# Kernel optimization log

Hardware: AMD Instinct MI355X
Metric: run time of the kernel (lower is better)

Reference implementation:

```python
import jax, jax.numpy as jnp
import numpy as np

B = 256        # graphs
NODES = 116    # nodes per view per graph
FEAT = 115     # node feature dim
LENN = 6670    # edges per view per graph (116*115/2)
SEG2 = 13456   # raw edges per graph in input (2*LENN + 116 discarded)
HID = 128      # hidden_channels
HC = 512       # hc


def setup_inputs() -> dict:
    key = jax.random.key(0)
    ks = jax.random.split(key, 12)
    x = jax.random.normal(ks[0], (B * 2 * NODES, FEAT), jnp.float32)
    # per-graph edge layout: [6670 FC edges | 6670 SC edges | 116 dummy]
    off = (2 * NODES) * jnp.arange(B, dtype=jnp.int32)  # [B]
    fc = jax.random.randint(ks[1], (2, B, LENN), 0, NODES, dtype=jnp.int32) + off[None, :, None]
    sc = jax.random.randint(ks[2], (2, B, LENN), 0, NODES, dtype=jnp.int32) + off[None, :, None] + NODES
    dummy = jnp.zeros((2, B, SEG2 - 2 * LENN), jnp.int32) + off[None, :, None]
    edge_index = jnp.concatenate([fc, sc, dummy], axis=2).reshape(2, B * SEG2)
    edge_weight = jax.random.uniform(ks[3], (B * SEG2,), jnp.float32)
    batch = jnp.repeat(jnp.arange(B, dtype=jnp.int32), 2 * NODES)
    s = 1.0 / np.sqrt(FEAT)
    W1 = jax.random.uniform(ks[4], (FEAT, HID), jnp.float32, -s, s)
    b1 = jnp.zeros((HID,), jnp.float32)
    W2 = jax.random.uniform(ks[5], (FEAT, HID), jnp.float32, -s, s)
    b2 = jnp.zeros((HID,), jnp.float32)
    s6 = 1.0 / np.sqrt(2 * NODES)
    W6 = jax.random.uniform(ks[6], (2 * NODES, HC), jnp.float32, -s6, s6)
    b6 = jax.random.uniform(ks[7], (HC,), jnp.float32, -s6, s6)
    s7 = 1.0 / np.sqrt(HC)
    W7 = jax.random.uniform(ks[8], (HC, 1), jnp.float32, -s7, s7)
    b7 = jax.random.uniform(ks[9], (1,), jnp.float32, -s7, s7)
    return dict(x=x, edge_index=edge_index, edge_weight=edge_weight, batch=batch,
                W1=W1, b1=b1, W2=W2, b2=b2, W6=W6, b6=b6, W7=W7, b7=b7)


def _gcn_conv(x, ei, ew, W, b, num_nodes):
    """PyG GCNConv: D^-1/2 (A+I) D^-1/2 X W + b (self-loop weight 1)."""
    h = x @ W                                   # [N, HID]
    src, dst = ei[0], ei[1]
    deg = jax.ops.segment_sum(ew, dst, num_segments=num_nodes) + 1.0  # +1 self-loop
    dinv = jax.lax.rsqrt(deg)                   # [N]
    norm = dinv[src] * ew * dinv[dst]           # [E]
    out = jax.ops.segment_sum(h[src] * norm[:, None], dst, num_segments=num_nodes)
    out = out + (dinv * dinv)[:, None] * h      # self-loop message
    return out + b


def reference(x, edge_index, edge_weight, batch, W1, b1, W2, b2, W6, b6, W7, b7):
    gidx = jnp.arange(B, dtype=edge_index.dtype)
    ei = edge_index.reshape(2, B, SEG2)
    ew = edge_weight.reshape(B, SEG2)
    # de-offset per-graph edges into per-view node index spaces (116 nodes/graph)
    ei_fc = (ei[:, :, :LENN] - NODES * gidx[None, :, None]).reshape(2, B * LENN)
    ei_sc = (ei[:, :, LENN:2 * LENN] - NODES * (gidx + 1)[None, :, None]).reshape(2, B * LENN)
    ew_fc = ew[:, :LENN].reshape(-1)
    ew_sc = ew[:, LENN:2 * LENN].reshape(-1)
    xr = x.reshape(B, 2 * NODES, FEAT)
    node_fc = xr[:, :NODES].reshape(B * NODES, FEAT)
    node_sc = xr[:, NODES:].reshape(B * NODES, FEAT)
    N = B * NODES
    x1 = _gcn_conv(node_fc, ei_fc, ew_fc, W1, b1, N).max(axis=1)  # [B*116]
    x2 = _gcn_conv(node_sc, ei_sc, ew_sc, W2, b2, N).max(axis=1)  # [B*116]
    feat = jnp.stack([x1, x2], axis=1).reshape(B, 2 * NODES)      # flatten()
    # dropout p=0.5 is identity in eval mode
    h = jax.nn.relu(feat @ W6 + b6)
    return h @ W7 + b7  # [B, 1]
```

## Files before the change

kernel.cpp:

```cpp
#include <hip/hip_runtime.h>


#define NB 256
#define NODES 116
#define FEAT 115
#define LENN 6670
#define SEG2 13456
#define HID 128
#define HC 512
#define AF_STR 117

typedef float f32x4 __attribute__((ext_vector_type(4)));
typedef short short8 __attribute__((ext_vector_type(8)));
typedef __bf16 bf16x8 __attribute__((ext_vector_type(8)));

#define MFMA16(a, b, c) __builtin_amdgcn_mfma_f32_16x16x32_bf16( \
    __builtin_bit_cast(bf16x8, (a)), __builtin_bit_cast(bf16x8, (b)), (c), 0, 0, 0)

#define OFF_ALO 32768
#define OFF_BHI 65536
#define OFF_BLO 98304
#define OFF_PMAX 131072
#define OFF_DINV 133120
#define LDS_BYTES 133632

__device__ __forceinline__ unsigned short f2bf_s(float f) {
  return __builtin_bit_cast(unsigned short, (__bf16)f);
}
__device__ __forceinline__ float bf2f_s(unsigned short h) {
  return __builtin_bit_cast(float, (unsigned)h << 16);
}
__device__ __forceinline__ void cvt4(const float* v, uint2& hi, uint2& lo) {
  unsigned short h[4], l[4];
#pragma unroll
  for (int j = 0; j < 4; ++j) {
    h[j] = f2bf_s(v[j]);
    l[j] = f2bf_s(v[j] - bf2f_s(h[j]));
  }
  hi.x = (unsigned)h[0] | ((unsigned)h[1] << 16);
  hi.y = (unsigned)h[2] | ((unsigned)h[3] << 16);
  lo.x = (unsigned)l[0] | ((unsigned)l[1] << 16);
  lo.y = (unsigned)l[2] | ((unsigned)l[3] << 16);
}
__device__ __forceinline__ int kperm(int k) {
  return (k & ~31) | (k & 3) | (((k >> 2) & 3) << 3) | (((k >> 4) & 1) << 2);
}
__device__ __forceinline__ int kb64(int t) {
  return ((t & 3) << 4) | (((t >> 2) & 1) << 3) | ((t >> 3) << 6);
}
__device__ __forceinline__ int swzb(int row, int kbyte) {
  return row * 256 + (kbyte ^ ((row & 7) << 4));
}
__device__ __forceinline__ f32x4 splat4(float f) {
  f32x4 r = {f, f, f, f};
  return r;
}

__global__ __launch_bounds__(1024, 1) void k_fused(
    const float* __restrict__ x, const int* __restrict__ ei,
    const float* __restrict__ ew,
    const float* __restrict__ W1, const float* __restrict__ b1,
    const float* __restrict__ W2, const float* __restrict__ b2,
    float* __restrict__ featws)
{
  __shared__ __align__(16) char sm[LDS_BYTES];
  float* Afp   = (float*)(sm + OFF_BHI);
  float* dinv  = (float*)(sm + OFF_DINV);
  float* pmaxp = (float*)(sm + OFF_PMAX);
  const int bid = blockIdx.x;
  const int g = bid >> 1, v = bid & 1;
  const int tid = threadIdx.x;

  {
    f32x4 z = splat4(0.f);
    f32x4* p = (f32x4*)(sm + OFF_BHI);
    for (int i = tid; i < 3393; i += 1024) p[i] = z;
  }
  __syncthreads();

  const int eoff = g * SEG2 + v * LENN;
  const int nbase = g * 232 + v * 116;

  {
    const int* __restrict__ srcp = ei + eoff;
    const int* __restrict__ dstp = ei + (size_t)NB * SEG2 + eoff;
    const float* __restrict__ wp = ew + eoff;
    for (int q = tid; q < (LENN / 2); q += 1024) {
      int2 s2 = ((const int2*)srcp)[q];
      int2 d2 = ((const int2*)dstp)[q];
      float2 w2 = ((const float2*)wp)[q];
      atomicAdd(&Afp[(d2.x - nbase) * AF_STR + (s2.x - nbase)], w2.x);
      atomicAdd(&Afp[(d2.y - nbase) * AF_STR + (s2.y - nbase)], w2.y);
    }
  }
  __syncthreads();

  if (tid < 4 * NODES) {
    const int r = tid >> 2, q = tid & 3;
    const float* row = Afp + r * AF_STR + q * 29;
    float s = 0.f;
#pragma unroll
    for (int j = 0; j < 29; ++j) s += row[j];
    s += __shfl_xor(s, 1, 64);
    s += __shfl_xor(s, 2, 64);
    if (q == 0) dinv[r] = rsqrtf(s + 1.0f);
  }
  __syncthreads();

  float xr[4][4];
  {
    const float* __restrict__ xg = x + (size_t)nbase * FEAT;
#pragma unroll
    for (int i = 0; i < 4; ++i) {
      int u = tid + (i << 10);
      int t = u >> 7, c = u & 127;
#pragma unroll
      for (int j = 0; j < 4; ++j) {
        int s = 4 * t + j;
        xr[i][j] = (c < FEAT && s < NODES) ? xg[s * FEAT + c] : 0.f;
      }
    }
  }

  for (int p = tid; p < NODES * 32; p += 1024) {
    const int row = p >> 5;
    const int t = p & 31;
    const int c = t << 2;
    float tv[4] = {0.f, 0.f, 0.f, 0.f};
    if (t < 29) {
      const float dr = dinv[row];
#pragma unroll
      for (int j = 0; j < 4; ++j) {
        const int cc = c + j;
        float q = Afp[row * AF_STR + cc] * (dr * dinv[cc]);
        if (cc == row) q += dr * dr;
        tv[j] = q;
      }
    }
    uint2 hi, lo;
    cvt4(tv, hi, lo);
    const int byte = swzb(row, kb64(t));
    *(uint2*)(sm + byte) = hi;
    *(uint2*)(sm + OFF_ALO + byte) = lo;
  }
  __syncthreads();

#pragma unroll
  for (int i = 0; i < 4; ++i) {
    int u = tid + (i << 10);
    int t = u >> 7, c = u & 127;
    uint2 hi, lo;
    cvt4(xr[i], hi, lo);
    int byte = swzb(c, kb64(t));
    *(uint2*)(sm + OFF_BHI + byte) = hi;
    *(uint2*)(sm + OFF_BLO + byte) = lo;
  }
  __syncthreads();

  const int lane = tid & 63, w = tid >> 6;
  const int mg = w >> 2, ng = w & 3;
  const int rA0 = (mg << 5) + (lane & 15), rA1 = rA0 + 16;
  const int rB0 = (ng << 5) + (lane & 15), rB1 = rB0 + 16;
  const int kb = (lane >> 4) << 4;

  float wr[4][4];
  {
    const float* __restrict__ Wv = v ? W2 : W1;
#pragma unroll
    for (int i = 0; i < 4; ++i) {
      int u = tid + (i << 10);
      int t = u >> 7, c = u & 127;
#pragma unroll
      for (int j = 0; j < 4; ++j) {
        int k = 4 * t + j;
        wr[i][j] = (k < FEAT) ? Wv[(size_t)k * HID + c] : 0.f;
      }
    }
  }

  f32x4 acc00 = splat4(0.f), acc01 = splat4(0.f);
  f32x4 acc10 = splat4(0.f), acc11 = splat4(0.f);

#pragma unroll
  for (int kc = 0; kc < 4; ++kc) {
    const int ko = (kc << 6) + kb;
    short8 a0h = *(const short8*)(sm + swzb(rA0, ko));
    short8 a0l = *(const short8*)(sm + OFF_ALO + swzb(rA0, ko));
    short8 a1h = *(const short8*)(sm + swzb(rA1, ko));
    short8 a1l = *(const short8*)(sm + OFF_ALO + swzb(rA1, ko));
    short8 b0h = *(const short8*)(sm + OFF_BHI + swzb(rB0, ko));
    short8 b0l = *(const short8*)(sm + OFF_BLO + swzb(rB0, ko));
    short8 b1h = *(const short8*)(sm + OFF_BHI + swzb(rB1, ko));
    short8 b1l = *(const short8*)(sm + OFF_BLO + swzb(rB1, ko));
    acc00 = MFMA16(a0h, b0h, acc00); acc00 = MFMA16(a0l, b0h, acc00); acc00 = MFMA16(a0h, b0l, acc00);
    acc01 = MFMA16(a0h, b1h, acc01); acc01 = MFMA16(a0l, b1h, acc01); acc01 = MFMA16(a0h, b1l, acc01);
    acc10 = MFMA16(a1h, b0h, acc10); acc10 = MFMA16(a1l, b0h, acc10); acc10 = MFMA16(a1h, b0l, acc10);
    acc11 = MFMA16(a1h, b1h, acc11); acc11 = MFMA16(a1l, b1h, acc11); acc11 = MFMA16(a1h, b1l, acc11);
  }
  __syncthreads();

  {
#pragma unroll
    for (int mt = 0; mt < 2; ++mt)
#pragma unroll
      for (int nt = 0; nt < 2; ++nt)
#pragma unroll
        for (int r2 = 0; r2 < 4; ++r2) {
          f32x4 a = (mt == 0) ? (nt == 0 ? acc00 : acc01)
                              : (nt == 0 ? acc10 : acc11);
          float f = a[r2];
          int row = (mg << 5) + (mt << 4) + ((lane >> 4) << 2) + r2;
          int col = (ng << 5) + (nt << 4) + (lane & 15);
          unsigned short hi = f2bf_s(f);
          unsigned short lo = f2bf_s(f - bf2f_s(hi));
          int byte = swzb(row, kperm(col) << 1);
          *(unsigned short*)(sm + byte) = hi;
          *(unsigned short*)(sm + OFF_ALO + byte) = lo;
        }
#pragma unroll
    for (int i = 0; i < 4; ++i) {
      int u = tid + (i << 10);
      int t = u >> 7, c = u & 127;
      uint2 hi, lo;
      cvt4(wr[i], hi, lo);
      int byte = swzb(c, kb64(t));
      *(uint2*)(sm + OFF_BHI + byte) = hi;
      *(uint2*)(sm + OFF_BLO + byte) = lo;
    }
  }
  __syncthreads();

  {
    const float* __restrict__ bv = v ? b2 : b1;
    float bb0 = bv[(ng << 5) + (lane & 15)];
    float bb1 = bv[(ng << 5) + 16 + (lane & 15)];
    acc00 = splat4(bb0); acc01 = splat4(bb1);
    acc10 = splat4(bb0); acc11 = splat4(bb1);
  }
#pragma unroll
  for (int kc = 0; kc < 4; ++kc) {
    const int ko = (kc << 6) + kb;
    short8 a0h = *(const short8*)(sm + swzb(rA0, ko));
    short8 a0l = *(const short8*)(sm + OFF_ALO + swzb(rA0, ko));
    short8 a1h = *(const short8*)(sm + swzb(rA1, ko));
    short8 a1l = *(const short8*)(sm + OFF_ALO + swzb(rA1, ko));
    short8 b0h = *(const short8*)(sm + OFF_BHI + swzb(rB0, ko));
    short8 b0l = *(const short8*)(sm + OFF_BLO + swzb(rB0, ko));
    short8 b1h = *(const short8*)(sm + OFF_BHI + swzb(rB1, ko));
    short8 b1l = *(const short8*)(sm + OFF_BLO + swzb(rB1, ko));
    acc00 = MFMA16(a0h, b0h, acc00); acc00 = MFMA16(a0l, b0h, acc00); acc00 = MFMA16(a0h, b0l, acc00);
    acc01 = MFMA16(a0h, b1h, acc01); acc01 = MFMA16(a0l, b1h, acc01); acc01 = MFMA16(a0h, b1l, acc01);
    acc10 = MFMA16(a1h, b0h, acc10); acc10 = MFMA16(a1l, b0h, acc10); acc10 = MFMA16(a1h, b0l, acc10);
    acc11 = MFMA16(a1h, b1h, acc11); acc11 = MFMA16(a1l, b1h, acc11); acc11 = MFMA16(a1h, b1l, acc11);
  }

#pragma unroll
  for (int mt = 0; mt < 2; ++mt)
#pragma unroll
    for (int r2 = 0; r2 < 4; ++r2) {
      f32x4 aN0 = (mt == 0) ? acc00 : acc10;
      f32x4 aN1 = (mt == 0) ? acc01 : acc11;
      float m = fmaxf(aN0[r2], aN1[r2]);
      m = fmaxf(m, __shfl_xor(m, 1, 64));
      m = fmaxf(m, __shfl_xor(m, 2, 64));
      m = fmaxf(m, __shfl_xor(m, 4, 64));
      m = fmaxf(m, __shfl_xor(m, 8, 64));
      if ((lane & 15) == 0) {
        int row = (mg << 5) + (mt << 4) + ((lane >> 4) << 2) + r2;
        pmaxp[(ng << 7) + row] = m;
      }
    }
  __syncthreads();
  if (tid < NODES) {
    float m = fmaxf(fmaxf(pmaxp[tid], pmaxp[128 + tid]),
                    fmaxf(pmaxp[256 + tid], pmaxp[384 + tid]));
    featws[g * 232 + 2 * tid + v] = m;
  }
}

__global__ __launch_bounds__(1024) void k_mlp(
    const float* __restrict__ featws, const float* __restrict__ W6,
    const float* __restrict__ b6, const float* __restrict__ W7,
    const float* __restrict__ b7, float* __restrict__ out)
{
  __shared__ float sf[232];
  __shared__ float ph[512];
  __shared__ float red[8];
  const int g = blockIdx.x, tid = threadIdx.x;
  if (tid < 232) sf[tid] = featws[g * 232 + tid];
  __syncthreads();

  const int col = tid & 511, half = tid >> 9;
  const float* __restrict__ w6p = W6 + (size_t)(half * 116) * HC + col;
  const float* __restrict__ sfh = sf + half * 116;
  float p = 0.f;
#pragma unroll 4
  for (int k = 0; k < 116; ++k)
    p = fmaf(sfh[k], w6p[(size_t)k * HC], p);
  if (half) ph[col] = p;
  __syncthreads();

  if (!half) {
    float a = b6[col] + p + ph[col];
    a = fmaxf(a, 0.f) * W7[col];
#pragma unroll
    for (int off = 32; off >= 1; off >>= 1) a += __shfl_xor(a, off, 64);
    if ((tid & 63) == 0) red[tid >> 6] = a;
  }
  __syncthreads();
  if (tid == 0) {
    float t = b7[0];
#pragma unroll
    for (int i = 0; i < 8; ++i) t += red[i];
    out[g] = t;
  }
}

extern "C" void kernel_launch(void* const* d_in, const int* in_sizes, int n_in,
                              void* d_out, int out_size, void* d_ws, size_t ws_size,
                              hipStream_t stream)
{
  const float* x  = (const float*)d_in[0];
  const int*   ei = (const int*)d_in[1];
  const float* ew = (const float*)d_in[2];
  const float* W1 = (const float*)d_in[4];
  const float* b1 = (const float*)d_in[5];
  const float* W2 = (const float*)d_in[6];
  const float* b2 = (const float*)d_in[7];
  const float* W6 = (const float*)d_in[8];
  const float* b6 = (const float*)d_in[9];
  const float* W7 = (const float*)d_in[10];
  const float* b7 = (const float*)d_in[11];

  float* featws = (float*)d_ws;
  float* out    = (float*)d_out;

  hipLaunchKernelGGL(k_fused, dim3(2 * NB), dim3(1024), 0, stream,
                     x, ei, ew, W1, b1, W2, b2, featws);
  hipLaunchKernelGGL(k_mlp,   dim3(NB),     dim3(1024), 0, stream,
                     featws, W6, b6, W7, b7, out);
}
```

Baseline: 157.6 us.

## Fuse GCN and MLP into one kernel with one block per graph

```diff
diff --git a/kernel.cpp b/kernel.cpp
--- a/kernel.cpp
+++ b/kernel.cpp
@@ -8,7 +8,7 @@
 #define SEG2 13456
 #define HID 128
 #define HC 512
-#define AF_STR 117
+#define AF_STR 120
 
 typedef float f32x4 __attribute__((ext_vector_type(4)));
 typedef short short8 __attribute__((ext_vector_type(8)));
@@ -22,7 +22,9 @@
 #define OFF_BLO 98304
 #define OFF_PMAX 131072
 #define OFF_DINV 133120
-#define LDS_BYTES 133632
+#define OFF_FEAT 133632
+#define OFF_RED  134560
+#define LDS_BYTES 134592
 
 __device__ __forceinline__ unsigned short f2bf_s(float f) {
   return __builtin_bit_cast(unsigned short, (__bf16)f);
@@ -56,263 +58,257 @@
   return r;
 }
 
-__global__ __launch_bounds__(1024, 1) void k_fused(
+__global__ __launch_bounds__(1024, 1) void k_all(
     const float* __restrict__ x, const int* __restrict__ ei,
     const float* __restrict__ ew,
     const float* __restrict__ W1, const float* __restrict__ b1,
     const float* __restrict__ W2, const float* __restrict__ b2,
-    float* __restrict__ featws)
+    const float* __restrict__ W6, const float* __restrict__ b6,
+    const float* __restrict__ W7, const float* __restrict__ b7,
+    float* __restrict__ out)
 {
   __shared__ __align__(16) char sm[LDS_BYTES];
   float* Afp   = (float*)(sm + OFF_BHI);
   float* dinv  = (float*)(sm + OFF_DINV);
   float* pmaxp = (float*)(sm + OFF_PMAX);
-  const int bid = blockIdx.x;
-  const int g = bid >> 1, v = bid & 1;
+  float* sfeat = (float*)(sm + OFF_FEAT);
+  float* redp  = (float*)(sm + OFF_RED);
+  const int g = blockIdx.x;
   const int tid = threadIdx.x;
-
-  {
-    f32x4 z = splat4(0.f);
-    f32x4* p = (f32x4*)(sm + OFF_BHI);
-    for (int i = tid; i < 3393; i += 1024) p[i] = z;
-  }
-  __syncthreads();
-
-  const int eoff = g * SEG2 + v * LENN;
-  const int nbase = g * 232 + v * 116;
-
-  {
-    const int* __restrict__ srcp = ei + eoff;
-    const int* __restrict__ dstp = ei + (size_t)NB * SEG2 + eoff;
-    const float* __restrict__ wp = ew + eoff;
-    for (int q = tid; q < (LENN / 2); q += 1024) {
-      int2 s2 = ((const int2*)srcp)[q];
-      int2 d2 = ((const int2*)dstp)[q];
-      float2 w2 = ((const float2*)wp)[q];
-      atomicAdd(&Afp[(d2.x - nbase) * AF_STR + (s2.x - nbase)], w2.x);
-      atomicAdd(&Afp[(d2.y - nbase) * AF_STR + (s2.y - nbase)], w2.y);
-    }
-  }
-  __syncthreads();
-
-  if (tid < 4 * NODES) {
-    const int r = tid >> 2, q = tid & 3;
-    const float* row = Afp + r * AF_STR + q * 29;
-    float s = 0.f;
-#pragma unroll
-    for (int j = 0; j < 29; ++j) s += row[j];
-    s += __shfl_xor(s, 1, 64);
-    s += __shfl_xor(s, 2, 64);
-    if (q == 0) dinv[r] = rsqrtf(s + 1.0f);
-  }
-  __syncthreads();
-
-  float xr[4][4];
-  {
-    const float* __restrict__ xg = x + (size_t)nbase * FEAT;
-#pragma unroll
-    for (int i = 0; i < 4; ++i) {
-      int u = tid + (i << 10);
-      int t = u >> 7, c = u & 127;
-#pragma unroll
-      for (int j = 0; j < 4; ++j) {
-        int s = 4 * t + j;
-        xr[i][j] = (c < FEAT && s < NODES) ? xg[s * FEAT + c] : 0.f;
-      }
-    }
-  }
-
-  for (int p = tid; p < NODES * 32; p += 1024) {
-    const int row = p >> 5;
-    const int t = p & 31;
-    const int c = t << 2;
-    float tv[4] = {0.f, 0.f, 0.f, 0.f};
-    if (t < 29) {
-      const float dr = dinv[row];
-#pragma unroll
-      for (int j = 0; j < 4; ++j) {
-        const int cc = c + j;
-        float q = Afp[row * AF_STR + cc] * (dr * dinv[cc]);
-        if (cc == row) q += dr * dr;
-        tv[j] = q;
-      }
-    }
-    uint2 hi, lo;
-    cvt4(tv, hi, lo);
-    const int byte = swzb(row, kb64(t));
-    *(uint2*)(sm + byte) = hi;
-    *(uint2*)(sm + OFF_ALO + byte) = lo;
-  }
-  __syncthreads();
-
-#pragma unroll
-  for (int i = 0; i < 4; ++i) {
-    int u = tid + (i << 10);
-    int t = u >> 7, c = u & 127;
-    uint2 hi, lo;
-    cvt4(xr[i], hi, lo);
-    int byte = swzb(c, kb64(t));
-    *(uint2*)(sm + OFF_BHI + byte) = hi;
-    *(uint2*)(sm + OFF_BLO + byte) = lo;
-  }
-  __syncthreads();
-
   const int lane = tid & 63, w = tid >> 6;
   const int mg = w >> 2, ng = w & 3;
   const int rA0 = (mg << 5) + (lane & 15), rA1 = rA0 + 16;
   const int rB0 = (ng << 5) + (lane & 15), rB1 = rB0 + 16;
   const int kb = (lane >> 4) << 4;
 
-  float wr[4][4];
-  {
-    const float* __restrict__ Wv = v ? W2 : W1;
-#pragma unroll
-    for (int i = 0; i < 4; ++i) {
-      int u = tid + (i << 10);
-      int t = u >> 7, c = u & 127;
-#pragma unroll
-      for (int j = 0; j < 4; ++j) {
-        int k = 4 * t + j;
-        wr[i][j] = (k < FEAT) ? Wv[(size_t)k * HID + c] : 0.f;
-      }
-    }
-  }
-
-  f32x4 acc00 = splat4(0.f), acc01 = splat4(0.f);
-  f32x4 acc10 = splat4(0.f), acc11 = splat4(0.f);
-
-#pragma unroll
-  for (int kc = 0; kc < 4; ++kc) {
-    const int ko = (kc << 6) + kb;
-    short8 a0h = *(const short8*)(sm + swzb(rA0, ko));
-    short8 a0l = *(const short8*)(sm + OFF_ALO + swzb(rA0, ko));
-    short8 a1h = *(const short8*)(sm + swzb(rA1, ko));
-    short8 a1l = *(const short8*)(sm + OFF_ALO + swzb(rA1, ko));
-    short8 b0h = *(const short8*)(sm + OFF_BHI + swzb(rB0, ko));
-    short8 b0l = *(const short8*)(sm + OFF_BLO + swzb(rB0, ko));
-    short8 b1h = *(const short8*)(sm + OFF_BHI + swzb(rB1, ko));
-    short8 b1l = *(const short8*)(sm + OFF_BLO + swzb(rB1, ko));
-    acc00 = MFMA16(a0h, b0h, acc00); acc00 = MFMA16(a0l, b0h, acc00); acc00 = MFMA16(a0h, b0l, acc00);
-    acc01 = MFMA16(a0h, b1h, acc01); acc01 = MFMA16(a0l, b1h, acc01); acc01 = MFMA16(a0h, b1l, acc01);
-    acc10 = MFMA16(a1h, b0h, acc10); acc10 = MFMA16(a1l, b0h, acc10); acc10 = MFMA16(a1h, b0l, acc10);
-    acc11 = MFMA16(a1h, b1h, acc11); acc11 = MFMA16(a1l, b1h, acc11); acc11 = MFMA16(a1h, b1l, acc11);
-  }
-  __syncthreads();
-
-  {
-#pragma unroll
-    for (int mt = 0; mt < 2; ++mt)
-#pragma unroll
-      for (int nt = 0; nt < 2; ++nt)
-#pragma unroll
-        for (int r2 = 0; r2 < 4; ++r2) {
-          f32x4 a = (mt == 0) ? (nt == 0 ? acc00 : acc01)
-                              : (nt == 0 ? acc10 : acc11);
-          float f = a[r2];
-          int row = (mg << 5) + (mt << 4) + ((lane >> 4) << 2) + r2;
-          int col = (ng << 5) + (nt << 4) + (lane & 15);
-          unsigned short hi = f2bf_s(f);
-          unsigned short lo = f2bf_s(f - bf2f_s(hi));
-          int byte = swzb(row, kperm(col) << 1);
-          *(unsigned short*)(sm + byte) = hi;
-          *(unsigned short*)(sm + OFF_ALO + byte) = lo;
+  for (int v = 0; v < 2; ++v) {
+    {
+      f32x4 z = splat4(0.f);
+      f32x4* p = (f32x4*)(sm + OFF_BHI);
+      for (int i = tid; i < 3480; i += 1024) p[i] = z;
+    }
+    __syncthreads();
+
+    const int eoff = g * SEG2 + v * LENN;
+    const int nbase = g * 232 + v * 116;
+
+    {
+      const int* __restrict__ srcp = ei + eoff;
+      const int* __restrict__ dstp = ei + (size_t)NB * SEG2 + eoff;
+      const float* __restrict__ wp = ew + eoff;
+      for (int q = tid; q < (LENN / 2); q += 1024) {
+        int2 s2 = ((const int2*)srcp)[q];
+        int2 d2 = ((const int2*)dstp)[q];
+        float2 w2 = ((const float2*)wp)[q];
+        atomicAdd(&Afp[(d2.x - nbase) * AF_STR + (s2.x - nbase)], w2.x);
+        atomicAdd(&Afp[(d2.y - nbase) * AF_STR + (s2.y - nbase)], w2.y);
+      }
+    }
+    __syncthreads();
+
+    if (tid < 4 * NODES) {
+      const int r = tid >> 2, q = tid & 3;
+      const float* row = Afp + r * AF_STR + q * 29;
+      float s = 0.f;
+#pragma unroll
+      for (int j = 0; j < 29; ++j) s += row[j];
+      s += __shfl_xor(s, 1, 64);
+      s += __shfl_xor(s, 2, 64);
+      if (q == 0) dinv[r] = rsqrtf(s + 1.0f);
+    }
+    __syncthreads();
+
+    float xr[4][4];
+    {
+      const float* __restrict__ xg = x + (size_t)nbase * FEAT;
+#pragma unroll
+      for (int i = 0; i < 4; ++i) {
+        int u = tid + (i << 10);
+        int t = u >> 7, c = u & 127;
+#pragma unroll
+        for (int j = 0; j < 4; ++j) {
+          int s = 4 * t + j;
+          xr[i][j] = (c < FEAT && s < NODES) ? xg[s * FEAT + c] : 0.f;
         }
+      }
+    }
+
+    for (int p = tid; p < NODES * 32; p += 1024) {
+      const int row = p >> 5;
+      const int t = p & 31;
+      float tv[4] = {0.f, 0.f, 0.f, 0.f};
+      if (t < 29) {
+        const float dr = dinv[row];
+        f32x4 q4 = *(const f32x4*)(Afp + row * AF_STR + (t << 2));
+#pragma unroll
+        for (int j = 0; j < 4; ++j) {
+          const int cc = (t << 2) + j;
+          float q = q4[j] * (dr * dinv[cc]);
+          if (cc == row) q += dr * dr;
+          tv[j] = q;
+        }
+      }
+      uint2 hi, lo;
+      cvt4(tv, hi, lo);
+      const int byte = swzb(row, kb64(t));
+      *(uint2*)(sm + byte) = hi;
+      *(uint2*)(sm + OFF_ALO + byte) = lo;
+    }
+    __syncthreads();
+
 #pragma unroll
     for (int i = 0; i < 4; ++i) {
       int u = tid + (i << 10);
       int t = u >> 7, c = u & 127;
       uint2 hi, lo;
-      cvt4(wr[i], hi, lo);
+      cvt4(xr[i], hi, lo);
       int byte = swzb(c, kb64(t));
       *(uint2*)(sm + OFF_BHI + byte) = hi;
       *(uint2*)(sm + OFF_BLO + byte) = lo;
     }
+    __syncthreads();
+
+    float wr[4][4];
+    {
+      const float* __restrict__ Wv = v ? W2 : W1;
+#pragma unroll
+      for (int i = 0; i < 4; ++i) {
+        int u = tid + (i << 10);
+        int t = u >> 7, c = u & 127;
+#pragma unroll
+        for (int j = 0; j < 4; ++j) {
+          int k = 4 * t + j;
+          wr[i][j] = (k < FEAT) ? Wv[(size_t)k * HID + c] : 0.f;
+        }
+      }
+    }
+
+    f32x4 acc00 = splat4(0.f), acc01 = splat4(0.f);
+    f32x4 acc10 = splat4(0.f), acc11 = splat4(0.f);
+
+#pragma unroll
+    for (int kc = 0; kc < 4; ++kc) {
+      const int ko = (kc << 6) + kb;
+      short8 a0h = *(const short8*)(sm + swzb(rA0, ko));
+      short8 a0l = *(const short8*)(sm + OFF_ALO + swzb(rA0, ko));
+      short8 a1h = *(const short8*)(sm + swzb(rA1, ko));
+      short8 a1l = *(const short8*)(sm + OFF_ALO + swzb(rA1, ko));
+      short8 b0h = *(const short8*)(sm + OFF_BHI + swzb(rB0, ko));
+      short8 b0l = *(const short8*)(sm + OFF_BLO + swzb(rB0, ko));
+      short8 b1h = *(const short8*)(sm + OFF_BHI + swzb(rB1, ko));
+      short8 b1l = *(const short8*)(sm + OFF_BLO + swzb(rB1, ko));
+      acc00 = MFMA16(a0h, b0h, acc00); acc00 = MFMA16(a0l, b0h, acc00); acc00 = MFMA16(a0h, b0l, acc00);
+      acc01 = MFMA16(a0h, b1h, acc01); acc01 = MFMA16(a0l, b1h, acc01); acc01 = MFMA16(a0h, b1l, acc01);
+      acc10 = MFMA16(a1h, b0h, acc10); acc10 = MFMA16(a1l, b0h, acc10); acc10 = MFMA16(a1h, b0l, acc10);
+      acc11 = MFMA16(a1h, b1h, acc11); acc11 = MFMA16(a1l, b1h, acc11); acc11 = MFMA16(a1h, b1l, acc11);
+    }
+    __syncthreads();
+
+    {
+#pragma unroll
+      for (int mt = 0; mt < 2; ++mt)
+#pragma unroll
+        for (int nt = 0; nt < 2; ++nt)
+#pragma unroll
+          for (int r2 = 0; r2 < 4; ++r2) {
+            f32x4 a = (mt == 0) ? (nt == 0 ? acc00 : acc01)
+                                : (nt == 0 ? acc10 : acc11);
+            float f = a[r2];
+            int row = (mg << 5) + (mt << 4) + ((lane >> 4) << 2) + r2;
+            int col = (ng << 5) + (nt << 4) + (lane & 15);
+            unsigned short hi = f2bf_s(f);
+            unsigned short lo = f2bf_s(f - bf2f_s(hi));
+            int byte = swzb(row, kperm(col) << 1);
+            *(unsigned short*)(sm + byte) = hi;
+            *(unsigned short*)(sm + OFF_ALO + byte) = lo;
+          }
+#pragma unroll
+      for (int i = 0; i < 4; ++i) {
+        int u = tid + (i << 10);
+        int t = u >> 7, c = u & 127;
+        uint2 hi, lo;
+        cvt4(wr[i], hi, lo);
+        int byte = swzb(c, kb64(t));
+        *(uint2*)(sm + OFF_BHI + byte) = hi;
+        *(uint2*)(sm + OFF_BLO + byte) = lo;
+      }
+    }
+    __syncthreads();
+
+    {
+      const float* __restrict__ bv = v ? b2 : b1;
+      float bb0 = bv[(ng << 5) + (lane & 15)];
+      float bb1 = bv[(ng << 5) + 16 + (lane & 15)];
+      acc00 = splat4(bb0); acc01 = splat4(bb1);
+      acc10 = splat4(bb0); acc11 = splat4(bb1);
+    }
+#pragma unroll
+    for (int kc = 0; kc < 4; ++kc) {
+      const int ko = (kc << 6) + kb;
+      short8 a0h = *(const short8*)(sm + swzb(rA0, ko));
+      short8 a0l = *(const short8*)(sm + OFF_ALO + swzb(rA0, ko));
+      short8 a1h = *(const short8*)(sm + swzb(rA1, ko));
+      short8 a1l = *(const short8*)(sm + OFF_ALO + swzb(rA1, ko));
+      short8 b0h = *(const short8*)(sm + OFF_BHI + swzb(rB0, ko));
+      short8 b0l = *(const short8*)(sm + OFF_BLO + swzb(rB0, ko));
+      short8 b1h = *(const short8*)(sm + OFF_BHI + swzb(rB1, ko));
+      short8 b1l = *(const short8*)(sm + OFF_BLO + swzb(rB1, ko));
+      acc00 = MFMA16(a0h, b0h, acc00); acc00 = MFMA16(a0l, b0h, acc00); acc00 = MFMA16(a0h, b0l, acc00);
+      acc01 = MFMA16(a0h, b1h, acc01); acc01 = MFMA16(a0l, b1h, acc01); acc01 = MFMA16(a0h, b1l, acc01);
+      acc10 = MFMA16(a1h, b0h, acc10); acc10 = MFMA16(a1l, b0h, acc10); acc10 = MFMA16(a1h, b0l, acc10);
+      acc11 = MFMA16(a1h, b1h, acc11); acc11 = MFMA16(a1l, b1h, acc11); acc11 = MFMA16(a1h, b1l, acc11);
+    }
+
+#pragma unroll
+    for (int mt = 0; mt < 2; ++mt)
+#pragma unroll
+      for (int r2 = 0; r2 < 4; ++r2) {
+        f32x4 aN0 = (mt == 0) ? acc00 : acc10;
+        f32x4 aN1 = (mt == 0) ? acc01 : acc11;
+        float m = fmaxf(aN0[r2], aN1[r2]);
+        m = fmaxf(m, __shfl_xor(m, 1, 64));
+        m = fmaxf(m, __shfl_xor(m, 2, 64));
+        m = fmaxf(m, __shfl_xor(m, 4, 64));
+        m = fmaxf(m, __shfl_xor(m, 8, 64));
+        if ((lane & 15) == 0) {
+          int row = (mg << 5) + (mt << 4) + ((lane >> 4) << 2) + r2;
+          pmaxp[(ng << 7) + row] = m;
+        }
+      }
+    __syncthreads();
+    if (tid < NODES) {
+      float m = fmaxf(fmaxf(pmaxp[tid], pmaxp[128 + tid]),
+                      fmaxf(pmaxp[256 + tid], pmaxp[384 + tid]));
+      sfeat[2 * tid + v] = m;
+    }
+    __syncthreads();
   }
-  __syncthreads();
 
   {
-    const float* __restrict__ bv = v ? b2 : b1;
-    float bb0 = bv[(ng << 5) + (lane & 15)];
-    float bb1 = bv[(ng << 5) + 16 + (lane & 15)];
-    acc00 = splat4(bb0); acc01 = splat4(bb1);
-    acc10 = splat4(bb0); acc11 = splat4(bb1);
-  }
-#pragma unroll
-  for (int kc = 0; kc < 4; ++kc) {
-    const int ko = (kc << 6) + kb;
-    short8 a0h = *(const short8*)(sm + swzb(rA0, ko));
-    short8 a0l = *(const short8*)(sm + OFF_ALO + swzb(rA0, ko));
-    short8 a1h = *(const short8*)(sm + swzb(rA1, ko));
-    short8 a1l = *(const short8*)(sm + OFF_ALO + swzb(rA1, ko));
-    short8 b0h = *(const short8*)(sm + OFF_BHI + swzb(rB0, ko));
-    short8 b0l = *(const short8*)(sm + OFF_BLO + swzb(rB0, ko));
-    short8 b1h = *(const short8*)(sm + OFF_BHI + swzb(rB1, ko));
-    short8 b1l = *(const short8*)(sm + OFF_BLO + swzb(rB1, ko));
-    acc00 = MFMA16(a0h, b0h, acc00); acc00 = MFMA16(a0l, b0h, acc00); acc00 = MFMA16(a0h, b0l, acc00);
-    acc01 = MFMA16(a0h, b1h, acc01); acc01 = MFMA16(a0l, b1h, acc01); acc01 = MFMA16(a0h, b1l, acc01);
-    acc10 = MFMA16(a1h, b0h, acc10); acc10 = MFMA16(a1l, b0h, acc10); acc10 = MFMA16(a1h, b0l, acc10);
-    acc11 = MFMA16(a1h, b1h, acc11); acc11 = MFMA16(a1l, b1h, acc11); acc11 = MFMA16(a1h, b1l, acc11);
-  }
-
-#pragma unroll
-  for (int mt = 0; mt < 2; ++mt)
-#pragma unroll
-    for (int r2 = 0; r2 < 4; ++r2) {
-      f32x4 aN0 = (mt == 0) ? acc00 : acc10;
-      f32x4 aN1 = (mt == 0) ? acc01 : acc11;
-      float m = fmaxf(aN0[r2], aN1[r2]);
-      m = fmaxf(m, __shfl_xor(m, 1, 64));
-      m = fmaxf(m, __shfl_xor(m, 2, 64));
-      m = fmaxf(m, __shfl_xor(m, 4, 64));
-      m = fmaxf(m, __shfl_xor(m, 8, 64));
-      if ((lane & 15) == 0) {
-        int row = (mg << 5) + (mt << 4) + ((lane >> 4) << 2) + r2;
-        pmaxp[(ng << 7) + row] = m;
-      }
-    }
-  __syncthreads();
-  if (tid < NODES) {
-    float m = fmaxf(fmaxf(pmaxp[tid], pmaxp[128 + tid]),
-                    fmaxf(pmaxp[256 + tid], pmaxp[384 + tid]));
-    featws[g * 232 + 2 * tid + v] = m;
-  }
-}
-
-__global__ __launch_bounds__(1024) void k_mlp(
-    const float* __restrict__ featws, const float* __restrict__ W6,
-    const float* __restrict__ b6, const float* __restrict__ W7,
-    const float* __restrict__ b7, float* __restrict__ out)
-{
-  __shared__ float sf[232];
-  __shared__ float ph[512];
-  __shared__ float red[8];
-  const int g = blockIdx.x, tid = threadIdx.x;
-  if (tid < 232) sf[tid] = featws[g * 232 + tid];
-  __syncthreads();
-
-  const int col = tid & 511, half = tid >> 9;
-  const float* __restrict__ w6p = W6 + (size_t)(half * 116) * HC + col;
-  const float* __restrict__ sfh = sf + half * 116;
-  float p = 0.f;
+    const int col = tid & 511, half = tid >> 9;
+    const float* __restrict__ w6p = W6 + (size_t)(half * 116) * HC + col;
+    const float* __restrict__ sfh = sfeat + half * 116;
+    float p = 0.f;
 #pragma unroll 4
-  for (int k = 0; k < 116; ++k)
-    p = fmaf(sfh[k], w6p[(size_t)k * HC], p);
-  if (half) ph[col] = p;
-  __syncthreads();
-
-  if (!half) {
-    float a = b6[col] + p + ph[col];
-    a = fmaxf(a, 0.f) * W7[col];
-#pragma unroll
-    for (int off = 32; off >= 1; off >>= 1) a += __shfl_xor(a, off, 64);
-    if ((tid & 63) == 0) red[tid >> 6] = a;
-  }
-  __syncthreads();
-  if (tid == 0) {
-    float t = b7[0];
-#pragma unroll
-    for (int i = 0; i < 8; ++i) t += red[i];
-    out[g] = t;
+    for (int k = 0; k < 116; ++k)
+      p = fmaf(sfh[k], w6p[(size_t)k * HC], p);
+    float* ph = pmaxp;
+    if (half) ph[col] = p;
+    __syncthreads();
+    if (!half) {
+      float a = b6[col] + p + ph[col];
+      a = fmaxf(a, 0.f) * W7[col];
+#pragma unroll
+      for (int off = 32; off >= 1; off >>= 1) a += __shfl_xor(a, off, 64);
+      if ((tid & 63) == 0) redp[tid >> 6] = a;
+    }
+    __syncthreads();
+    if (tid == 0) {
+      float t = b7[0];
+#pragma unroll
+      for (int i = 0; i < 8; ++i) t += redp[i];
+      out[g] = t;
+    }
   }
 }
 
@@ -331,12 +327,8 @@
   const float* b6 = (const float*)d_in[9];
   const float* W7 = (const float*)d_in[10];
   const float* b7 = (const float*)d_in[11];
-
-  float* featws = (float*)d_ws;
-  float* out    = (float*)d_out;
-
-  hipLaunchKernelGGL(k_fused, dim3(2 * NB), dim3(1024), 0, stream,
-                     x, ei, ew, W1, b1, W2, b2, featws);
-  hipLaunchKernelGGL(k_mlp,   dim3(NB),     dim3(1024), 0, stream,
-                     featws, W6, b6, W7, b7, out);
-}
+  float* out = (float*)d_out;
+
+  hipLaunchKernelGGL(k_all, dim3(NB), dim3(1024), 0, stream,
+                     x, ei, ew, W1, b1, W2, b2, W6, b6, W7, b7, out);
+}
```

Measured after the change: 207.2 us. +31.4%, slower.
